# Kernel tuning notes

Measured on AMD Instinct MI355X. Metric: run time of the kernel, lower is better.

The kernel has to match this reference:

```python
import jax, jax.numpy as jnp
import numpy as np

DIM = 128
WS = 8            # window_size
NH = 4            # num_heads
SHIFT = 4         # shift_size
HD = DIM // NH    # head_dim = 32
SCALE = HD ** (-0.5)
N = WS * WS       # tokens per window = 64


def _rel_pos_index():
    # Static relative-position index, [N, N], values in [0, (2*WS-1)^2)
    coords = np.stack(np.meshgrid(np.arange(WS), np.arange(WS), indexing='ij'))  # [2,WS,WS]
    cf = coords.reshape(2, -1)                                                   # [2,N]
    rel = (cf[:, :, None] - cf[:, None, :]).transpose(1, 2, 0)                   # [N,N,2]
    rel[:, :, 0] += WS - 1
    rel[:, :, 1] += WS - 1
    rel[:, :, 0] *= 2 * WS - 1
    return rel.sum(-1)


def _shift_mask(H, W):
    # Static shifted-window attention mask, [nW, N, N] with 0 / -100 entries
    img = np.zeros((H, W))
    cnt = 0
    for hs in (slice(0, -WS), slice(-WS, -SHIFT), slice(-SHIFT, None)):
        for ws in (slice(0, -WS), slice(-WS, -SHIFT), slice(-SHIFT, None)):
            img[hs, ws] = cnt
            cnt += 1
    mw = img.reshape(H // WS, WS, W // WS, WS).transpose(0, 2, 1, 3).reshape(-1, N)
    am = mw[:, None, :] - mw[:, :, None]
    return np.where(am != 0, -100.0, 0.0).astype(np.float32)


def setup_inputs() -> dict:
    key = jax.random.key(0)
    ks = jax.random.split(key, 5)
    B, H, W = 8, 256, 256
    x = jax.random.normal(ks[0], (B, DIM, H, W), dtype=jnp.float32)
    qkv_w = jax.random.normal(ks[1], (3 * DIM, DIM), dtype=jnp.float32) * (DIM ** -0.5)
    proj_w = jax.random.normal(ks[2], (DIM, DIM), dtype=jnp.float32) * (DIM ** -0.5)
    proj_b = jax.random.normal(ks[3], (DIM,), dtype=jnp.float32) * 0.01
    bias_table = jax.random.normal(ks[4], ((2 * WS - 1) ** 2, NH), dtype=jnp.float32) * 0.02
    return {"x": x, "qkv_w": qkv_w, "proj_w": proj_w, "proj_b": proj_b,
            "bias_table": bias_table}


def reference(x, qkv_w, proj_w, proj_b, bias_table):
    B, C, H, W = x.shape
    # cyclic shift
    x = jnp.roll(x, (-SHIFT, -SHIFT), axis=(2, 3))
    # 1x1 conv qkv == channel matmul
    qkv = jnp.einsum('bchw,oc->bohw', x, qkv_w)  # [B, 3C, H, W]
    nWh, nWw = H // WS, W // WS
    nW = nWh * nWw
    qkv = qkv.reshape(B, 3, NH, HD, nWh, WS, nWw, WS)
    qkv = qkv.transpose(1, 0, 4, 6, 2, 5, 7, 3)          # [3,B,nWh,nWw,NH,WS,WS,HD]
    qkv = qkv.reshape(3, B * nW, NH, N, HD)
    q, k, v = qkv[0], qkv[1], qkv[2]
    attn = jnp.einsum('wnqd,wnkd->wnqk', q, k) * SCALE   # [B*nW, NH, N, N]
    # relative position bias gather
    rpi = _rel_pos_index().reshape(-1)
    bias = bias_table[rpi].reshape(N, N, NH).transpose(2, 0, 1)  # [NH,N,N]
    attn = attn + bias[None]
    # shifted-window mask
    mask = jnp.asarray(_shift_mask(H, W))                # [nW, N, N]
    attn = attn.reshape(B, nW, NH, N, N) + mask[None, :, None]
    attn = jax.nn.softmax(attn, axis=-1).reshape(B * nW, NH, N, N)
    out = jnp.einsum('wnqk,wnkd->wnqd', attn, v)         # [B*nW, NH, N, HD]
    out = out.reshape(B, nWh, nWw, NH, WS, WS, HD)
    out = out.transpose(0, 3, 6, 1, 4, 2, 5).reshape(B, C, H, W)
    out = jnp.einsum('bchw,oc->bohw', out, proj_w) + proj_b[None, :, None, None]
    out = jnp.roll(out, (SHIFT, SHIFT), axis=(2, 3))
    return out
```

## Files before the change

### kernel.cpp

```cpp
#include <hip/hip_runtime.h>

typedef __attribute__((ext_vector_type(8))) short short8;
typedef __attribute__((ext_vector_type(4))) unsigned short ushort4v;
typedef __attribute__((ext_vector_type(4))) float f32x4;

#define SCALE_F 0.17677669529663687f
#define SW(t) ((((t) ^ ((t) >> 3)) & 7) << 4)

__device__ __forceinline__ unsigned short f2bf(float f){
  unsigned u = __builtin_bit_cast(unsigned, f);
  u += 0x7fffu + ((u >> 16) & 1u);
  return (unsigned short)(u >> 16);
}
__device__ __forceinline__ float bf2f(unsigned short h){
  unsigned u = ((unsigned)h) << 16;
  return __builtin_bit_cast(float, u);
}
__device__ __forceinline__ unsigned cvtpk(float a, float b){
  unsigned w;
  asm("v_cvt_pk_bf16_f32 %0, %1, %2" : "=v"(w) : "v"(a), "v"(b));
  return w;
}
__device__ __forceinline__ void st_pk4(void* p, f32x4 a){
  uint2 u; u.x = cvtpk(a[0], a[1]); u.y = cvtpk(a[2], a[3]);
  *(uint2*)p = u;
}


template<bool WSB>
__global__ void __launch_bounds__(256, 2)
swin_fused(const float* __restrict__ x, const float* __restrict__ qkvw_f,
           const float* __restrict__ projw_f, const float* __restrict__ projb,
           const float* __restrict__ btab, const unsigned short* __restrict__ wbf,
           float* __restrict__ out)
{
  __shared__ __align__(16) unsigned char sm[65536];
  const int tid  = threadIdx.x;
  const int lane = tid & 63, wv = tid >> 6;
  const int lr = lane & 15, lg = lane >> 4;

  const int bid = blockIdx.x;
  const int sw  = ((bid & 7) << 10) | (bid >> 3);
  const int b   = sw >> 10;
  const int wh  = (sw >> 5) & 31, ww = sw & 31;
  const int hb  = wh * 8 + 4, wb = ww * 8 + 4;
  const bool h31 = (wh == 31), w31 = (ww == 31);

  short8 BwH[2][4];
  float pbH[2];
  #pragma unroll
  for (int ntl = 0; ntl < 2; ++ntl) {
    const int o = (wv + 4 * ntl) * 16 + lr;
    pbH[ntl] = projb[o];
    #pragma unroll
    for (int kk = 0; kk < 4; ++kk) {
      const int off = o * 128 + kk * 32 + 8 * lg;
      if constexpr (WSB) {
        BwH[ntl][kk] = *(const short8*)(wbf + 49152 + off);
      } else {
        const float* p = projw_f + off;
        short8 r;
        #pragma unroll
        for (int e = 0; e < 8; ++e) r[e] = (short)f2bf(p[e]);
        BwH[ntl][kk] = r;
      }
    }
  }

  {
    #pragma unroll
    for (int it = 0; it < 8; ++it) {
      const int f = tid + 256 * it;
      const int c    = f >> 4;
      const int rr   = (f >> 1) & 7;
      const int half = f & 1;
      const int gh = (hb + rr) & 255;
      const int gw = (wb + 4 * half) & 255;
      const f32x4 v = *(const f32x4*)(x + (((b * 128 + c) << 16) + (gh << 8) + gw));
      const int t0 = rr * 8 + 4 * half;
      #pragma unroll
      for (int e = 0; e < 4; ++e) {
        const int t = t0 + e;
        *(unsigned short*)(sm + t * 256 + ((2 * c) ^ SW(t))) = f2bf(v[e]);
      }
    }
  }
  __syncthreads();

  {
    short8 Bf[16];
    #pragma unroll
    for (int nt = 0; nt < 4; ++nt)
      #pragma unroll
      for (int kk = 0; kk < 4; ++kk) {
        const int t = nt * 16 + lr;
        Bf[nt * 4 + kk] = *(short8*)(sm + t * 256 + ((64 * kk + 16 * lg) ^ SW(t)));
      }
    #pragma unroll
    for (int jj = 0; jj < 6; ++jj) {
      const int mt = wv + 4 * jj;
      const int orow = mt * 16 + lr;
      short8 Af[4];
      #pragma unroll
      for (int kk = 0; kk < 4; ++kk) {
        const int off = orow * 128 + kk * 32 + 8 * lg;
        if constexpr (WSB) {
          Af[kk] = *(const short8*)(wbf + off);
        } else {
          const float* p = qkvw_f + off;
          short8 r;
          #pragma unroll
          for (int e = 0; e < 8; ++e) r[e] = (short)f2bf(p[e]);
          Af[kk] = r;
        }
      }
      f32x4 acc[4];
      #pragma unroll
      for (int nt = 0; nt < 4; ++nt) {
        acc[nt] = (f32x4)(0.f);
        #pragma unroll
        for (int kk = 0; kk < 4; ++kk)
          acc[nt] = __builtin_amdgcn_mfma_f32_16x16x32_bf16(Af[kk], Bf[nt * 4 + kk], acc[nt], 0, 0, 0);
      }
      if (mt < 16) {
        const int base = (mt < 8) ? 16384 : 32768;
        const int c0 = ((mt & 7) * 16) + 4 * lg;
        #pragma unroll
        for (int nt = 0; nt < 4; ++nt) {
          const int t = nt * 16 + lr;
          ushort4v pk;
          #pragma unroll
          for (int r = 0; r < 4; ++r) pk[r] = f2bf(acc[nt][r]);
          *(ushort4v*)(sm + base + t * 256 + ((2 * c0) ^ SW(t))) = pk;
        }
      } else {
        const int c0 = (mt - 16) * 16 + 4 * lg;
        #pragma unroll
        for (int nt = 0; nt < 4; ++nt) {
          const int t = nt * 16 + lr;
          #pragma unroll
          for (int r = 0; r < 4; ++r) {
            const int c = c0 + r;
            *(unsigned short*)(sm + 49152 + c * 128 + ((2 * t) ^ SW(c))) = f2bf(acc[nt][r]);
          }
        }
      }
    }
  }
  __syncthreads();

  const int ktc = wv * 16 + lr;
  const int ki = ktc >> 3, kj = ktc & 7;
  int boff[4][4];
  #pragma unroll
  for (int mt = 0; mt < 4; ++mt)
    #pragma unroll
    for (int r = 0; r < 4; ++r) {
      const int qrow = mt * 16 + 4 * lg + r;
      boff[mt][r] = (((qrow >> 3) - ki + 7) * 15 + ((qrow & 7) - kj + 7)) * 4;
    }

  f32x4 accpv[8];
  #pragma unroll
  for (int z = 0; z < 8; ++z) accpv[z] = (f32x4)(0.f);

  #pragma unroll 1
  for (int h = 0; h < 4; ++h) {
    {
      const int cb = 64 * h + 16 * lg;
      const short8 kb = *(short8*)(sm + 32768 + ktc * 256 + (cb ^ SW(ktc)));
      #pragma unroll
      for (int mt = 0; mt < 4; ++mt) {
        const int q = mt * 16 + lr;
        const short8 qa = *(short8*)(sm + 16384 + q * 256 + (cb ^ SW(q)));
        f32x4 sacc = __builtin_amdgcn_mfma_f32_16x16x32_bf16(qa, kb, (f32x4)(0.f), 0, 0, 0);
        #pragma unroll
        for (int r = 0; r < 4; ++r) {
          const int qrow = mt * 16 + 4 * lg + r;
          float s = sacc[r] * SCALE_F;
          s += btab[boff[mt][r] + h];
          if (h31 | w31) {
            const int qi = qrow >> 3, qj = qrow & 7;
            const bool bad = (h31 && ((qi >= 4) != (ki >= 4))) ||
                             (w31 && ((qj >= 4) != (kj >= 4)));
            s += bad ? -100.f : 0.f;
          }
          *(unsigned short*)(sm + qrow * 128 + ((2 * ktc) ^ SW(qrow))) = f2bf(s);
        }
      }
    }
    __syncthreads();
    {
      const int srow = tid >> 2, sq = tid & 3;
      const int swz = SW(srow);
      const short8 s0 = *(short8*)(sm + srow * 128 + ((sq * 32) ^ swz));
      const short8 s1 = *(short8*)(sm + srow * 128 + ((sq * 32 + 16) ^ swz));
      float v[16];
      #pragma unroll
      for (int e = 0; e < 8; ++e) { v[e] = bf2f((unsigned short)s0[e]); v[e + 8] = bf2f((unsigned short)s1[e]); }
      float mx = v[0];
      #pragma unroll
      for (int e = 1; e < 16; ++e) mx = fmaxf(mx, v[e]);
      mx = fmaxf(mx, __shfl_xor(mx, 1));
      mx = fmaxf(mx, __shfl_xor(mx, 2));
      float sum = 0.f;
      #pragma unroll
      for (int e = 0; e < 16; ++e) { v[e] = __expf(v[e] - mx); sum += v[e]; }
      sum += __shfl_xor(sum, 1);
      sum += __shfl_xor(sum, 2);
      const float inv = 1.f / sum;
      short8 p0, p1;
      #pragma unroll
      for (int e = 0; e < 8; ++e) { p0[e] = (short)f2bf(v[e] * inv); p1[e] = (short)f2bf(v[e + 8] * inv); }
      *(short8*)(sm + 8192 + srow * 128 + ((sq * 32) ^ swz)) = p0;
      *(short8*)(sm + 8192 + srow * 128 + ((sq * 32 + 16) ^ swz)) = p1;
    }
    __syncthreads();
    {
      const int q = wv * 16 + lr;
      const short8 pa0 = *(short8*)(sm + 8192 + q * 128 + ((16 * lg) ^ SW(q)));
      const short8 pa1 = *(short8*)(sm + 8192 + q * 128 + ((64 + 16 * lg) ^ SW(q)));
      #pragma unroll
      for (int nd = 0; nd < 2; ++nd) {
        const int c = h * 32 + nd * 16 + lr;
        const short8 vb0 = *(short8*)(sm + 49152 + c * 128 + ((16 * lg) ^ SW(c)));
        const short8 vb1 = *(short8*)(sm + 49152 + c * 128 + ((64 + 16 * lg) ^ SW(c)));
        f32x4 a = accpv[h * 2 + nd];
        a = __builtin_amdgcn_mfma_f32_16x16x32_bf16(pa0, vb0, a, 0, 0, 0);
        a = __builtin_amdgcn_mfma_f32_16x16x32_bf16(pa1, vb1, a, 0, 0, 0);
        accpv[h * 2 + nd] = a;
      }
    }
  }

  {
    #pragma unroll
    for (int h = 0; h < 4; ++h)
      #pragma unroll
      for (int nd = 0; nd < 2; ++nd) {
        const int c = h * 32 + nd * 16 + lr;
        const f32x4 a = accpv[h * 2 + nd];
        #pragma unroll
        for (int r = 0; r < 4; ++r) {
          const int t = wv * 16 + 4 * lg + r;
          *(unsigned short*)(sm + 16384 + t * 256 + ((2 * c) ^ SW(t))) = f2bf(a[r]);
        }
      }
  }
  __syncthreads();

  {
    short8 Aa[16];
    #pragma unroll
    for (int mt = 0; mt < 4; ++mt)
      #pragma unroll
      for (int kk = 0; kk < 4; ++kk) {
        const int t = mt * 16 + lr;
        Aa[mt * 4 + kk] = *(short8*)(sm + 16384 + t * 256 + ((64 * kk + 16 * lg) ^ SW(t)));
      }
    #pragma unroll
    for (int ntl = 0; ntl < 2; ++ntl) {
      const int o = (wv + 4 * ntl) * 16 + lr;
      const float pb = pbH[ntl];
      #pragma unroll
      for (int mt = 0; mt < 4; ++mt) {
        f32x4 acc = (f32x4)(0.f);
        #pragma unroll
        for (int kk = 0; kk < 4; ++kk)
          acc = __builtin_amdgcn_mfma_f32_16x16x32_bf16(Aa[mt * 4 + kk], BwH[ntl][kk], acc, 0, 0, 0);
        const int t0 = mt * 16 + 4 * lg;
        const int gh = (hb + (t0 >> 3)) & 255;
        const int gw0 = (wb + (t0 & 7)) & 255;
        f32x4 ov;
        ov[0] = acc[0] + pb; ov[1] = acc[1] + pb; ov[2] = acc[2] + pb; ov[3] = acc[3] + pb;
        *(f32x4*)(out + (((b * 128 + o) << 16) + (gh << 8) + gw0)) = ov;
      }
    }
  }
}

__global__ void prep_weights(const float* __restrict__ qw, const float* __restrict__ pw,
                             unsigned short* __restrict__ wsb)
{
  const int i = blockIdx.x * 256 + threadIdx.x;
  const int idx = i * 4;
  const float* src = (idx < 49152) ? (qw + idx) : (pw + (idx - 49152));
  f32x4 v = *(const f32x4*)src;
  ushort4v o;
  #pragma unroll
  for (int e = 0; e < 4; ++e) o[e] = f2bf(v[e]);
  *(ushort4v*)(wsb + idx) = o;
}

extern "C" void kernel_launch(void* const* d_in, const int* in_sizes, int n_in,
                              void* d_out, int out_size, void* d_ws, size_t ws_size,
                              hipStream_t stream) {
  const float* x     = (const float*)d_in[0];
  const float* qkvw  = (const float*)d_in[1];
  const float* projw = (const float*)d_in[2];
  const float* projb = (const float*)d_in[3];
  const float* btab  = (const float*)d_in[4];
  float* out = (float*)d_out;

  if (ws_size >= 131072) {
    unsigned short* wsb = (unsigned short*)d_ws;
    prep_weights<<<64, 256, 0, stream>>>(qkvw, projw, wsb);
    swin_fused<true><<<8192, 256, 0, stream>>>(x, qkvw, projw, projb, btab, wsb, out);
  } else {
    swin_fused<false><<<8192, 256, 0, stream>>>(x, qkvw, projw, projb, btab, nullptr, out);
  }
}
```

Baseline: 415.8 us.

## Double block to 512 threads, processing two heads in parallel per window

Raises threads per block from 256 to 512 so each window uses 8 waves. Work is split so that wave pairs handle two heads at once, each with its own score buffer, and the loop shrinks from four head iterations to two. The QKV and projection GEMMs are redistributed so each wave does fewer tiles. The softmax now writes probabilities in place with packed bf16 conversion, and the projection input is staged at a different LDS offset. This cuts per-wave serial work and register pressure, at the cost of an extra barrier per iteration. With 64KB LDS per block, occupancy stays limited to few blocks per CU.

```diff
diff --git a/kernel.cpp b/kernel.cpp
--- a/kernel.cpp
+++ b/kernel.cpp
@@ -21,14 +21,10 @@
   asm("v_cvt_pk_bf16_f32 %0, %1, %2" : "=v"(w) : "v"(a), "v"(b));
   return w;
 }
-__device__ __forceinline__ void st_pk4(void* p, f32x4 a){
-  uint2 u; u.x = cvtpk(a[0], a[1]); u.y = cvtpk(a[2], a[3]);
-  *(uint2*)p = u;
-}
 
 
 template<bool WSB>
-__global__ void __launch_bounds__(256, 2)
+__global__ void __launch_bounds__(512, 4)
 swin_fused(const float* __restrict__ x, const float* __restrict__ qkvw_f,
            const float* __restrict__ projw_f, const float* __restrict__ projb,
            const float* __restrict__ btab, const unsigned short* __restrict__ wbf,
@@ -46,31 +42,27 @@
   const int hb  = wh * 8 + 4, wb = ww * 8 + 4;
   const bool h31 = (wh == 31), w31 = (ww == 31);
 
-  short8 BwH[2][4];
-  float pbH[2];
+  short8 BwH[4];
+  const int oP = wv * 16 + lr;
+  const float pbH = projb[oP];
   #pragma unroll
-  for (int ntl = 0; ntl < 2; ++ntl) {
-    const int o = (wv + 4 * ntl) * 16 + lr;
-    pbH[ntl] = projb[o];
-    #pragma unroll
-    for (int kk = 0; kk < 4; ++kk) {
-      const int off = o * 128 + kk * 32 + 8 * lg;
-      if constexpr (WSB) {
-        BwH[ntl][kk] = *(const short8*)(wbf + 49152 + off);
-      } else {
-        const float* p = projw_f + off;
-        short8 r;
-        #pragma unroll
-        for (int e = 0; e < 8; ++e) r[e] = (short)f2bf(p[e]);
-        BwH[ntl][kk] = r;
-      }
+  for (int kk = 0; kk < 4; ++kk) {
+    const int off = oP * 128 + kk * 32 + 8 * lg;
+    if constexpr (WSB) {
+      BwH[kk] = *(const short8*)(wbf + 49152 + off);
+    } else {
+      const float* p = projw_f + off;
+      short8 r;
+      #pragma unroll
+      for (int e = 0; e < 8; ++e) r[e] = (short)f2bf(p[e]);
+      BwH[kk] = r;
     }
   }
 
   {
     #pragma unroll
-    for (int it = 0; it < 8; ++it) {
-      const int f = tid + 256 * it;
+    for (int it = 0; it < 4; ++it) {
+      const int f = tid + 512 * it;
       const int c    = f >> 4;
       const int rr   = (f >> 1) & 7;
       const int half = f & 1;
@@ -96,24 +88,24 @@
         const int t = nt * 16 + lr;
         Bf[nt * 4 + kk] = *(short8*)(sm + t * 256 + ((64 * kk + 16 * lg) ^ SW(t)));
       }
-    #pragma unroll
-    for (int jj = 0; jj < 6; ++jj) {
-      const int mt = wv + 4 * jj;
-      const int orow = mt * 16 + lr;
+    auto ldw = [&](int orow, int kk) -> short8 {
+      const int off = orow * 128 + kk * 32 + 8 * lg;
+      if constexpr (WSB) {
+        return *(const short8*)(wbf + off);
+      } else {
+        const float* p = qkvw_f + off;
+        short8 r;
+        #pragma unroll
+        for (int e = 0; e < 8; ++e) r[e] = (short)f2bf(p[e]);
+        return r;
+      }
+    };
+    #pragma unroll
+    for (int sec = 0; sec < 3; ++sec) {
+      const int orow = (8 * sec + wv) * 16 + lr;
       short8 Af[4];
       #pragma unroll
-      for (int kk = 0; kk < 4; ++kk) {
-        const int off = orow * 128 + kk * 32 + 8 * lg;
-        if constexpr (WSB) {
-          Af[kk] = *(const short8*)(wbf + off);
-        } else {
-          const float* p = qkvw_f + off;
-          short8 r;
-          #pragma unroll
-          for (int e = 0; e < 8; ++e) r[e] = (short)f2bf(p[e]);
-          Af[kk] = r;
-        }
-      }
+      for (int kk = 0; kk < 4; ++kk) Af[kk] = ldw(orow, kk);
       f32x4 acc[4];
       #pragma unroll
       for (int nt = 0; nt < 4; ++nt) {
@@ -122,9 +114,9 @@
         for (int kk = 0; kk < 4; ++kk)
           acc[nt] = __builtin_amdgcn_mfma_f32_16x16x32_bf16(Af[kk], Bf[nt * 4 + kk], acc[nt], 0, 0, 0);
       }
-      if (mt < 16) {
-        const int base = (mt < 8) ? 16384 : 32768;
-        const int c0 = ((mt & 7) * 16) + 4 * lg;
+      if (sec < 2) {
+        const int base = (sec == 0) ? 16384 : 32768;
+        const int c0 = wv * 16 + 4 * lg;
         #pragma unroll
         for (int nt = 0; nt < 4; ++nt) {
           const int t = nt * 16 + lr;
@@ -134,7 +126,7 @@
           *(ushort4v*)(sm + base + t * 256 + ((2 * c0) ^ SW(t))) = pk;
         }
       } else {
-        const int c0 = (mt - 16) * 16 + 4 * lg;
+        const int c0 = wv * 16 + 4 * lg;
         #pragma unroll
         for (int nt = 0; nt < 4; ++nt) {
           const int t = nt * 16 + lr;
@@ -149,7 +141,9 @@
   }
   __syncthreads();
 
-  const int ktc = wv * 16 + lr;
+  const int hpar = wv >> 2;
+  const int wt   = wv & 3;
+  const int ktc = wt * 16 + lr;
   const int ki = ktc >> 3, kj = ktc & 7;
   int boff[4][4];
   #pragma unroll
@@ -159,13 +153,15 @@
       const int qrow = mt * 16 + 4 * lg + r;
       boff[mt][r] = (((qrow >> 3) - ki + 7) * 15 + ((qrow & 7) - kj + 7)) * 4;
     }
-
-  f32x4 accpv[8];
+  const int Sbase = 8192 * hpar;
+
+  f32x4 accpv[4];
   #pragma unroll
-  for (int z = 0; z < 8; ++z) accpv[z] = (f32x4)(0.f);
+  for (int z = 0; z < 4; ++z) accpv[z] = (f32x4)(0.f);
 
   #pragma unroll 1
-  for (int h = 0; h < 4; ++h) {
+  for (int p = 0; p < 2; ++p) {
+    const int h = 2 * p + hpar;
     {
       const int cb = 64 * h + 16 * lg;
       const short8 kb = *(short8*)(sm + 32768 + ktc * 256 + (cb ^ SW(ktc)));
@@ -185,16 +181,20 @@
                              (w31 && ((qj >= 4) != (kj >= 4)));
             s += bad ? -100.f : 0.f;
           }
-          *(unsigned short*)(sm + qrow * 128 + ((2 * ktc) ^ SW(qrow))) = f2bf(s);
+          *(unsigned short*)(sm + Sbase + qrow * 128 + ((2 * ktc) ^ SW(qrow))) = f2bf(s);
         }
       }
     }
     __syncthreads();
     {
       const int srow = tid >> 2, sq = tid & 3;
-      const int swz = SW(srow);
-      const short8 s0 = *(short8*)(sm + srow * 128 + ((sq * 32) ^ swz));
-      const short8 s1 = *(short8*)(sm + srow * 128 + ((sq * 32 + 16) ^ swz));
+      const int rrow = srow & 63;
+      unsigned char* const rp = sm + (srow >> 6) * 8192 + rrow * 128;
+      const int swz = SW(rrow);
+      const int o0 = (sq * 32) ^ swz;
+      const int o1 = (sq * 32 + 16) ^ swz;
+      const short8 s0 = *(short8*)(rp + o0);
+      const short8 s1 = *(short8*)(rp + o1);
       float v[16];
       #pragma unroll
       for (int e = 0; e < 8; ++e) { v[e] = bf2f((unsigned short)s0[e]); v[e + 8] = bf2f((unsigned short)s1[e]); }
@@ -209,41 +209,47 @@
       sum += __shfl_xor(sum, 1);
       sum += __shfl_xor(sum, 2);
       const float inv = 1.f / sum;
-      short8 p0, p1;
-      #pragma unroll
-      for (int e = 0; e < 8; ++e) { p0[e] = (short)f2bf(v[e] * inv); p1[e] = (short)f2bf(v[e + 8] * inv); }
-      *(short8*)(sm + 8192 + srow * 128 + ((sq * 32) ^ swz)) = p0;
-      *(short8*)(sm + 8192 + srow * 128 + ((sq * 32 + 16) ^ swz)) = p1;
+      uint2 w0, w1;
+      w0.x = cvtpk(v[0] * inv,  v[1] * inv);  w0.y = cvtpk(v[2] * inv,  v[3] * inv);
+      w1.x = cvtpk(v[4] * inv,  v[5] * inv);  w1.y = cvtpk(v[6] * inv,  v[7] * inv);
+      *(uint2*)(rp + o0) = w0;
+      *(uint2*)(rp + o0 + 8) = w1;
+      uint2 w2, w3;
+      w2.x = cvtpk(v[8] * inv,  v[9] * inv);  w2.y = cvtpk(v[10] * inv, v[11] * inv);
+      w3.x = cvtpk(v[12] * inv, v[13] * inv); w3.y = cvtpk(v[14] * inv, v[15] * inv);
+      *(uint2*)(rp + o1) = w2;
+      *(uint2*)(rp + o1 + 8) = w3;
     }
     __syncthreads();
     {
-      const int q = wv * 16 + lr;
-      const short8 pa0 = *(short8*)(sm + 8192 + q * 128 + ((16 * lg) ^ SW(q)));
-      const short8 pa1 = *(short8*)(sm + 8192 + q * 128 + ((64 + 16 * lg) ^ SW(q)));
+      const int q = wt * 16 + lr;
+      const short8 pa0 = *(short8*)(sm + Sbase + q * 128 + ((16 * lg) ^ SW(q)));
+      const short8 pa1 = *(short8*)(sm + Sbase + q * 128 + ((64 + 16 * lg) ^ SW(q)));
       #pragma unroll
       for (int nd = 0; nd < 2; ++nd) {
-        const int c = h * 32 + nd * 16 + lr;
+        const int c = 32 * h + nd * 16 + lr;
         const short8 vb0 = *(short8*)(sm + 49152 + c * 128 + ((16 * lg) ^ SW(c)));
         const short8 vb1 = *(short8*)(sm + 49152 + c * 128 + ((64 + 16 * lg) ^ SW(c)));
-        f32x4 a = accpv[h * 2 + nd];
+        f32x4 a = accpv[2 * p + nd];
         a = __builtin_amdgcn_mfma_f32_16x16x32_bf16(pa0, vb0, a, 0, 0, 0);
         a = __builtin_amdgcn_mfma_f32_16x16x32_bf16(pa1, vb1, a, 0, 0, 0);
-        accpv[h * 2 + nd] = a;
-      }
-    }
+        accpv[2 * p + nd] = a;
+      }
+    }
+    __syncthreads();
   }
 
   {
     #pragma unroll
-    for (int h = 0; h < 4; ++h)
+    for (int p = 0; p < 2; ++p)
       #pragma unroll
       for (int nd = 0; nd < 2; ++nd) {
-        const int c = h * 32 + nd * 16 + lr;
-        const f32x4 a = accpv[h * 2 + nd];
+        const int c = 32 * (2 * p + hpar) + nd * 16 + lr;
+        const f32x4 a = accpv[2 * p + nd];
         #pragma unroll
         for (int r = 0; r < 4; ++r) {
-          const int t = wv * 16 + 4 * lg + r;
-          *(unsigned short*)(sm + 16384 + t * 256 + ((2 * c) ^ SW(t))) = f2bf(a[r]);
+          const int t = wt * 16 + 4 * lg + r;
+          *(unsigned short*)(sm + 49152 + t * 256 + ((2 * c) ^ SW(t))) = f2bf(a[r]);
         }
       }
   }
@@ -256,25 +262,20 @@
       #pragma unroll
       for (int kk = 0; kk < 4; ++kk) {
         const int t = mt * 16 + lr;
-        Aa[mt * 4 + kk] = *(short8*)(sm + 16384 + t * 256 + ((64 * kk + 16 * lg) ^ SW(t)));
-      }
-    #pragma unroll
-    for (int ntl = 0; ntl < 2; ++ntl) {
-      const int o = (wv + 4 * ntl) * 16 + lr;
-      const float pb = pbH[ntl];
-      #pragma unroll
-      for (int mt = 0; mt < 4; ++mt) {
-        f32x4 acc = (f32x4)(0.f);
-        #pragma unroll
-        for (int kk = 0; kk < 4; ++kk)
-          acc = __builtin_amdgcn_mfma_f32_16x16x32_bf16(Aa[mt * 4 + kk], BwH[ntl][kk], acc, 0, 0, 0);
-        const int t0 = mt * 16 + 4 * lg;
-        const int gh = (hb + (t0 >> 3)) & 255;
-        const int gw0 = (wb + (t0 & 7)) & 255;
-        f32x4 ov;
-        ov[0] = acc[0] + pb; ov[1] = acc[1] + pb; ov[2] = acc[2] + pb; ov[3] = acc[3] + pb;
-        *(f32x4*)(out + (((b * 128 + o) << 16) + (gh << 8) + gw0)) = ov;
-      }
+        Aa[mt * 4 + kk] = *(short8*)(sm + 49152 + t * 256 + ((64 * kk + 16 * lg) ^ SW(t)));
+      }
+    #pragma unroll
+    for (int mt = 0; mt < 4; ++mt) {
+      f32x4 acc = (f32x4)(0.f);
+      #pragma unroll
+      for (int kk = 0; kk < 4; ++kk)
+        acc = __builtin_amdgcn_mfma_f32_16x16x32_bf16(Aa[mt * 4 + kk], BwH[kk], acc, 0, 0, 0);
+      const int t0 = mt * 16 + 4 * lg;
+      const int gh = (hb + (t0 >> 3)) & 255;
+      const int gw0 = (wb + (t0 & 7)) & 255;
+      f32x4 ov;
+      ov[0] = acc[0] + pbH; ov[1] = acc[1] + pbH; ov[2] = acc[2] + pbH; ov[3] = acc[3] + pbH;
+      *(f32x4*)(out + (((b * 128 + oP) << 16) + (gh << 8) + gw0)) = ov;
     }
   }
 }
@@ -305,8 +306,8 @@
   if (ws_size >= 131072) {
     unsigned short* wsb = (unsigned short*)d_ws;
     prep_weights<<<64, 256, 0, stream>>>(qkvw, projw, wsb);
-    swin_fused<true><<<8192, 256, 0, stream>>>(x, qkvw, projw, projb, btab, wsb, out);
+    swin_fused<true><<<8192, 512, 0, stream>>>(x, qkvw, projw, projb, btab, wsb, out);
   } else {
-    swin_fused<false><<<8192, 256, 0, stream>>>(x, qkvw, projw, projb, btab, nullptr, out);
-  }
-}
+    swin_fused<false><<<8192, 512, 0, stream>>>(x, qkvw, projw, projb, btab, nullptr, out);
+  }
+}
```

Result: slower. 624.5 us (+50.2%).

## Split fused Swin attention into compute kernel plus coalesced output scatter kernel

Applied to the files above, without the earlier changes.

Adds a two-kernel path for when the workspace is large enough. The first kernel does the QKV projection, windowed attention and output projection using a smaller LDS footprint (about 39 KB, launch bounds for 4 blocks per CU). It writes bf16 results per window into scratch. The second kernel reads that scratch and writes full, coalesced fp32 output rows with the cyclic roll applied. The aim is higher occupancy and better-coalesced stores than the fused kernel, at the cost of an extra scratch write and read plus bf16 rounding of the output.

```diff
diff --git a/kernel.cpp b/kernel.cpp
--- a/kernel.cpp
+++ b/kernel.cpp
@@ -3,6 +3,7 @@
 typedef __attribute__((ext_vector_type(8))) short short8;
 typedef __attribute__((ext_vector_type(4))) unsigned short ushort4v;
 typedef __attribute__((ext_vector_type(4))) float f32x4;
+typedef __attribute__((ext_vector_type(4))) unsigned int uint4v;
 
 #define SCALE_F 0.17677669529663687f
 #define SW(t) ((((t) ^ ((t) >> 3)) & 7) << 4)
@@ -26,6 +27,259 @@
   *(uint2*)p = u;
 }
 
+__global__ void prep_weights(const float* __restrict__ qw, const float* __restrict__ pw,
+                             unsigned short* __restrict__ wsb)
+{
+  const int i = blockIdx.x * 256 + threadIdx.x;
+  const int idx = i * 4;
+  const float* src = (idx < 49152) ? (qw + idx) : (pw + (idx - 49152));
+  f32x4 v = *(const f32x4*)src;
+  ushort4v o;
+  #pragma unroll
+  for (int e = 0; e < 4; ++e) o[e] = f2bf(v[e]);
+  *(ushort4v*)(wsb + idx) = o;
+}
+
+__global__ void __launch_bounds__(256, 4)
+swin_k1(const float* __restrict__ x, const float* __restrict__ projb,
+        const float* __restrict__ btab, const unsigned short* __restrict__ wbf,
+        unsigned short* __restrict__ scr)
+{
+  __shared__ __align__(16) unsigned char sm[39424];
+  unsigned char* const smq = sm + 16384;
+  unsigned char* const smk = sm + 21504;
+  unsigned char* const smv = sm + 26624;
+  unsigned char* const smS = sm + 31232;
+
+  const int tid  = threadIdx.x;
+  const int lane = tid & 63, wv = tid >> 6;
+  const int lr = lane & 15, lg = lane >> 4;
+
+  const int bid = blockIdx.x;
+  const int sw  = ((bid & 7) << 10) | (bid >> 3);
+  const int b   = sw >> 10;
+  const int wh  = (sw >> 5) & 31, ww = sw & 31;
+  const int hb  = wh * 8 + 4, wb = ww * 8 + 4;
+  const bool h31 = (wh == 31), w31 = (ww == 31);
+  const int win = sw;
+
+  {
+    #pragma unroll
+    for (int it = 0; it < 8; ++it) {
+      const int f = tid + 256 * it;
+      const int c    = f >> 4;
+      const int rr   = (f >> 1) & 7;
+      const int half = f & 1;
+      const int gh = (hb + rr) & 255;
+      const int gw = (wb + 4 * half) & 255;
+      const f32x4 v = *(const f32x4*)(x + (((b * 128 + c) << 16) + (gh << 8) + gw));
+      const int t0 = rr * 8 + 4 * half;
+      #pragma unroll
+      for (int e = 0; e < 4; ++e) {
+        const int t = t0 + e;
+        *(unsigned short*)(sm + t * 256 + ((2 * c) ^ SW(t))) = f2bf(v[e]);
+      }
+    }
+  }
+  __syncthreads();
+
+  const int ktc = wv * 16 + lr;
+  const int ki = ktc >> 3, kj = ktc & 7;
+  int boff[4][4];
+  #pragma unroll
+  for (int mt = 0; mt < 4; ++mt)
+    #pragma unroll
+    for (int r = 0; r < 4; ++r) {
+      const int qrow = mt * 16 + 4 * lg + r;
+      boff[mt][r] = (((qrow >> 3) - ki + 7) * 15 + ((qrow & 7) - kj + 7)) * 4;
+    }
+
+  f32x4 accpv[8];
+  #pragma unroll
+  for (int z = 0; z < 8; ++z) accpv[z] = (f32x4)(0.f);
+
+  auto ldx = [&](int t, int kk) -> short8 {
+    return *(const short8*)(sm + t * 256 + ((64 * kk + 16 * lg) ^ SW(t)));
+  };
+  auto ldw8 = [&](int row, int kk) -> short8 {
+    return *(const short8*)(wbf + row * 128 + kk * 32 + 8 * lg);
+  };
+
+  #pragma unroll 1
+  for (int h = 0; h < 4; ++h) {
+    {
+      const int prow0 = ((wv < 2) ? 32 * h : 128 + 32 * h) + 16 * (wv & 1);
+      short8 Af[4];
+      #pragma unroll
+      for (int kk = 0; kk < 4; ++kk) Af[kk] = ldw8(prow0 + lr, kk);
+      unsigned char* const dst = (wv < 2) ? smq : smk;
+      #pragma unroll
+      for (int nt = 0; nt < 4; ++nt) {
+        const int t = nt * 16 + lr;
+        f32x4 acc = (f32x4)(0.f);
+        #pragma unroll
+        for (int kk = 0; kk < 4; ++kk)
+          acc = __builtin_amdgcn_mfma_f32_16x16x32_bf16(Af[kk], ldx(t, kk), acc, 0, 0, 0);
+        if (wv < 2) { acc[0] *= SCALE_F; acc[1] *= SCALE_F; acc[2] *= SCALE_F; acc[3] *= SCALE_F; }
+        st_pk4(dst + t * 80 + 32 * (wv & 1) + 8 * lg, acc);
+      }
+      const int vrow0 = 256 + 32 * h + 16 * (wv >> 1);
+      short8 Av[4];
+      #pragma unroll
+      for (int kk = 0; kk < 4; ++kk) Av[kk] = ldw8(vrow0 + lr, kk);
+      #pragma unroll
+      for (int ntl = 0; ntl < 2; ++ntl) {
+        const int t = (2 * (wv & 1) + ntl) * 16 + lr;
+        f32x4 acc = (f32x4)(0.f);
+        #pragma unroll
+        for (int kk = 0; kk < 4; ++kk)
+          acc = __builtin_amdgcn_mfma_f32_16x16x32_bf16(Av[kk], ldx(t, kk), acc, 0, 0, 0);
+        const int cb = 16 * (wv >> 1) + 4 * lg;
+        #pragma unroll
+        for (int r = 0; r < 4; ++r)
+          *(unsigned short*)(smv + (cb + r) * 144 + 2 * t) = f2bf(acc[r]);
+      }
+    }
+    __syncthreads();
+
+    {
+      const short8 kb = *(const short8*)(smk + ktc * 80 + 16 * lg);
+      #pragma unroll
+      for (int mt = 0; mt < 4; ++mt) {
+        const short8 qa = *(const short8*)(smq + (mt * 16 + lr) * 80 + 16 * lg);
+        const f32x4 s = __builtin_amdgcn_mfma_f32_16x16x32_bf16(qa, kb, (f32x4)(0.f), 0, 0, 0);
+        #pragma unroll
+        for (int r = 0; r < 4; ++r) {
+          const int qrow = mt * 16 + 4 * lg + r;
+          float val = s[r] + btab[boff[mt][r] + h];
+          if (h31 | w31) {
+            const int qi = qrow >> 3, qj = qrow & 7;
+            const bool bad = (h31 && ((qi >= 4) != (ki >= 4))) ||
+                             (w31 && ((qj >= 4) != (kj >= 4)));
+            val += bad ? -100.f : 0.f;
+          }
+          *(unsigned short*)(smS + qrow * 128 + ((2 * ktc) ^ SW(qrow))) = f2bf(val);
+        }
+      }
+    }
+    __syncthreads();
+
+    {
+      const int srow = tid >> 2, sq = tid & 3;
+      unsigned char* const rp = smS + srow * 128;
+      const int o0 = (32 * sq) ^ SW(srow);
+      const int o1 = (32 * sq + 16) ^ SW(srow);
+      const short8 s0 = *(const short8*)(rp + o0);
+      const short8 s1 = *(const short8*)(rp + o1);
+      float v[16];
+      #pragma unroll
+      for (int e = 0; e < 8; ++e) { v[e] = bf2f((unsigned short)s0[e]); v[e + 8] = bf2f((unsigned short)s1[e]); }
+      float mx = v[0];
+      #pragma unroll
+      for (int e = 1; e < 16; ++e) mx = fmaxf(mx, v[e]);
+      mx = fmaxf(mx, __shfl_xor(mx, 1));
+      mx = fmaxf(mx, __shfl_xor(mx, 2));
+      float sum = 0.f;
+      #pragma unroll
+      for (int e = 0; e < 16; ++e) { v[e] = __expf(v[e] - mx); sum += v[e]; }
+      sum += __shfl_xor(sum, 1);
+      sum += __shfl_xor(sum, 2);
+      const float inv = 1.f / sum;
+      uint4v w0, w1;
+      w0.x = cvtpk(v[0] * inv, v[1] * inv);  w0.y = cvtpk(v[2] * inv, v[3] * inv);
+      w0.z = cvtpk(v[4] * inv, v[5] * inv);  w0.w = cvtpk(v[6] * inv, v[7] * inv);
+      w1.x = cvtpk(v[8] * inv, v[9] * inv);  w1.y = cvtpk(v[10] * inv, v[11] * inv);
+      w1.z = cvtpk(v[12] * inv, v[13] * inv); w1.w = cvtpk(v[14] * inv, v[15] * inv);
+      *(uint4v*)(rp + o0) = w0;
+      *(uint4v*)(rp + o1) = w1;
+    }
+    __syncthreads();
+
+    {
+      const int q = wv * 16 + lr;
+      const short8 pa0 = *(const short8*)(smS + q * 128 + ((16 * lg) ^ SW(q)));
+      const short8 pa1 = *(const short8*)(smS + q * 128 + ((64 + 16 * lg) ^ SW(q)));
+      #pragma unroll
+      for (int nd = 0; nd < 2; ++nd) {
+        const int c = nd * 16 + lr;
+        const short8 vb0 = *(const short8*)(smv + c * 144 + 16 * lg);
+        const short8 vb1 = *(const short8*)(smv + c * 144 + 64 + 16 * lg);
+        f32x4 a = accpv[2 * h + nd];
+        a = __builtin_amdgcn_mfma_f32_16x16x32_bf16(pa0, vb0, a, 0, 0, 0);
+        a = __builtin_amdgcn_mfma_f32_16x16x32_bf16(pa1, vb1, a, 0, 0, 0);
+        accpv[2 * h + nd] = a;
+      }
+    }
+    __syncthreads();
+  }
+
+  {
+    #pragma unroll
+    for (int h = 0; h < 4; ++h)
+      #pragma unroll
+      for (int nd = 0; nd < 2; ++nd) {
+        const int c = 32 * h + nd * 16 + lr;
+        const f32x4 a = accpv[2 * h + nd];
+        #pragma unroll
+        for (int r = 0; r < 4; ++r) {
+          const int t = wv * 16 + 4 * lg + r;
+          *(unsigned short*)(sm + t * 256 + ((2 * c) ^ SW(t))) = f2bf(a[r]);
+        }
+      }
+  }
+  __syncthreads();
+
+  {
+    short8 Aa[16];
+    #pragma unroll
+    for (int mt = 0; mt < 4; ++mt)
+      #pragma unroll
+      for (int kk = 0; kk < 4; ++kk) {
+        const int t = mt * 16 + lr;
+        Aa[mt * 4 + kk] = *(const short8*)(sm + t * 256 + ((64 * kk + 16 * lg) ^ SW(t)));
+      }
+    #pragma unroll
+    for (int ntl = 0; ntl < 2; ++ntl) {
+      const int o = (wv + 4 * ntl) * 16 + lr;
+      short8 Bw[4];
+      #pragma unroll
+      for (int kk = 0; kk < 4; ++kk)
+        Bw[kk] = *(const short8*)(wbf + 49152 + o * 128 + kk * 32 + 8 * lg);
+      const float pb = projb[o];
+      #pragma unroll
+      for (int mt = 0; mt < 4; ++mt) {
+        f32x4 acc = (f32x4)(0.f);
+        #pragma unroll
+        for (int kk = 0; kk < 4; ++kk)
+          acc = __builtin_amdgcn_mfma_f32_16x16x32_bf16(Aa[mt * 4 + kk], Bw[kk], acc, 0, 0, 0);
+        const int t0 = mt * 16 + 4 * lg;
+        uint2 u;
+        u.x = cvtpk(acc[0] + pb, acc[1] + pb);
+        u.y = cvtpk(acc[2] + pb, acc[3] + pb);
+        *(uint2*)(scr + ((win * 128 + o) << 6) + t0) = u;
+      }
+    }
+  }
+}
+
+__global__ void __launch_bounds__(256, 8)
+swin_k2(const unsigned short* __restrict__ scr, float* __restrict__ out)
+{
+  const int bid = blockIdx.x;
+  const int b = bid >> 12, whp = (bid >> 7) & 31, o = bid & 127;
+  const int tid = threadIdx.x;
+  const int gl = tid >> 5, l32 = tid & 31;
+  const int win = b * 1024 + whp * 32 + l32;
+  const short8 u = *(const short8*)(scr + ((win * 128 + o) << 6) + (gl << 3));
+  const int gh = (whp * 8 + 4 + gl) & 255;
+  float* const orow = out + (((b * 128 + o) << 16) + (gh << 8));
+  f32x4 v0, v1;
+  #pragma unroll
+  for (int e = 0; e < 4; ++e) { v0[e] = bf2f((unsigned short)u[e]); v1[e] = bf2f((unsigned short)u[e + 4]); }
+  const int gw0 = 8 * l32 + 4;
+  *(f32x4*)(orow + gw0) = v0;
+  *(f32x4*)(orow + ((gw0 + 4) & 255)) = v1;
+}
 
 template<bool WSB>
 __global__ void __launch_bounds__(256, 2)
@@ -279,19 +533,6 @@
   }
 }
 
-__global__ void prep_weights(const float* __restrict__ qw, const float* __restrict__ pw,
-                             unsigned short* __restrict__ wsb)
-{
-  const int i = blockIdx.x * 256 + threadIdx.x;
-  const int idx = i * 4;
-  const float* src = (idx < 49152) ? (qw + idx) : (pw + (idx - 49152));
-  f32x4 v = *(const f32x4*)src;
-  ushort4v o;
-  #pragma unroll
-  for (int e = 0; e < 4; ++e) o[e] = f2bf(v[e]);
-  *(ushort4v*)(wsb + idx) = o;
-}
-
 extern "C" void kernel_launch(void* const* d_in, const int* in_sizes, int n_in,
                               void* d_out, int out_size, void* d_ws, size_t ws_size,
                               hipStream_t stream) {
@@ -302,7 +543,14 @@
   const float* btab  = (const float*)d_in[4];
   float* out = (float*)d_out;
 
-  if (ws_size >= 131072) {
+  const size_t need_split = 131072u + (size_t)8192 * 8192 * 2;
+  if (ws_size >= need_split) {
+    unsigned short* wsb = (unsigned short*)d_ws;
+    unsigned short* scr = wsb + 65536;
+    prep_weights<<<64, 256, 0, stream>>>(qkvw, projw, wsb);
+    swin_k1<<<8192, 256, 0, stream>>>(x, projb, btab, wsb, scr);
+    swin_k2<<<32768, 256, 0, stream>>>(scr, out);
+  } else if (ws_size >= 131072) {
     unsigned short* wsb = (unsigned short*)d_ws;
     prep_weights<<<64, 256, 0, stream>>>(qkvw, projw, wsb);
     swin_fused<true><<<8192, 256, 0, stream>>>(x, qkvw, projw, projb, btab, wsb, out);
```

Result: slower. 561.5 us (+35.1%).

## Precompute dense bf16 bias table, defer proj weight loads, simplify LDS swizzle

Applied to the files above, without the earlier changes.

Adds a prep kernel that expands the relative-position bias into a dense bf16 [NH,64,64] table in workspace, so the attention loop reads bias by direct index instead of keeping a 16-entry offset array and doing a gather. Projection weights and bias are now loaded just before the output GEMM rather than held in registers for the whole kernel, which lowers register pressure. The LDS swizzle is simplified to use only the low row bits, and the head loop loses its no-unroll pragma. Risks: the new swizzle may cause more bank conflicts, bias values get bf16 rounding, and the workspace requirement grows.

```diff
diff --git a/kernel.cpp b/kernel.cpp
--- a/kernel.cpp
+++ b/kernel.cpp
@@ -5,7 +5,7 @@
 typedef __attribute__((ext_vector_type(4))) float f32x4;
 
 #define SCALE_F 0.17677669529663687f
-#define SW(t) ((((t) ^ ((t) >> 3)) & 7) << 4)
+#define SW(t) (((t) & 7) << 4)
 
 __device__ __forceinline__ unsigned short f2bf(float f){
   unsigned u = __builtin_bit_cast(unsigned, f);
@@ -16,16 +16,27 @@
   unsigned u = ((unsigned)h) << 16;
   return __builtin_bit_cast(float, u);
 }
-__device__ __forceinline__ unsigned cvtpk(float a, float b){
-  unsigned w;
-  asm("v_cvt_pk_bf16_f32 %0, %1, %2" : "=v"(w) : "v"(a), "v"(b));
-  return w;
-}
-__device__ __forceinline__ void st_pk4(void* p, f32x4 a){
-  uint2 u; u.x = cvtpk(a[0], a[1]); u.y = cvtpk(a[2], a[3]);
-  *(uint2*)p = u;
-}
-
+
+__global__ void prep_weights(const float* __restrict__ qw, const float* __restrict__ pw,
+                             unsigned short* __restrict__ wsb)
+{
+  const int i = blockIdx.x * 256 + threadIdx.x;
+  const int idx = i * 4;
+  const float* src = (idx < 49152) ? (qw + idx) : (pw + (idx - 49152));
+  f32x4 v = *(const f32x4*)src;
+  ushort4v o;
+  #pragma unroll
+  for (int e = 0; e < 4; ++e) o[e] = f2bf(v[e]);
+  *(ushort4v*)(wsb + idx) = o;
+}
+
+__global__ void prep_bias(const float* __restrict__ btab, unsigned short* __restrict__ biasb)
+{
+  const int idx = blockIdx.x * 256 + threadIdx.x;
+  const int h = idx >> 12, q = (idx >> 6) & 63, k = idx & 63;
+  const int rpi = ((q >> 3) - (k >> 3) + 7) * 15 + ((q & 7) - (k & 7) + 7);
+  biasb[idx] = f2bf(btab[rpi * 4 + h]);
+}
 
 template<bool WSB>
 __global__ void __launch_bounds__(256, 2)
@@ -46,27 +57,6 @@
   const int hb  = wh * 8 + 4, wb = ww * 8 + 4;
   const bool h31 = (wh == 31), w31 = (ww == 31);
 
-  short8 BwH[2][4];
-  float pbH[2];
-  #pragma unroll
-  for (int ntl = 0; ntl < 2; ++ntl) {
-    const int o = (wv + 4 * ntl) * 16 + lr;
-    pbH[ntl] = projb[o];
-    #pragma unroll
-    for (int kk = 0; kk < 4; ++kk) {
-      const int off = o * 128 + kk * 32 + 8 * lg;
-      if constexpr (WSB) {
-        BwH[ntl][kk] = *(const short8*)(wbf + 49152 + off);
-      } else {
-        const float* p = projw_f + off;
-        short8 r;
-        #pragma unroll
-        for (int e = 0; e < 8; ++e) r[e] = (short)f2bf(p[e]);
-        BwH[ntl][kk] = r;
-      }
-    }
-  }
-
   {
     #pragma unroll
     for (int it = 0; it < 8; ++it) {
@@ -152,19 +142,21 @@
   const int ktc = wv * 16 + lr;
   const int ki = ktc >> 3, kj = ktc & 7;
   int boff[4][4];
-  #pragma unroll
-  for (int mt = 0; mt < 4; ++mt)
-    #pragma unroll
-    for (int r = 0; r < 4; ++r) {
-      const int qrow = mt * 16 + 4 * lg + r;
-      boff[mt][r] = (((qrow >> 3) - ki + 7) * 15 + ((qrow & 7) - kj + 7)) * 4;
-    }
+  if constexpr (!WSB) {
+    #pragma unroll
+    for (int mt = 0; mt < 4; ++mt)
+      #pragma unroll
+      for (int r = 0; r < 4; ++r) {
+        const int qrow = mt * 16 + 4 * lg + r;
+        boff[mt][r] = (((qrow >> 3) - ki + 7) * 15 + ((qrow & 7) - kj + 7)) * 4;
+      }
+  }
+  const unsigned short* const biasb = WSB ? (wbf + 65536) : nullptr;
 
   f32x4 accpv[8];
   #pragma unroll
   for (int z = 0; z < 8; ++z) accpv[z] = (f32x4)(0.f);
 
-  #pragma unroll 1
   for (int h = 0; h < 4; ++h) {
     {
       const int cb = 64 * h + 16 * lg;
@@ -178,7 +170,11 @@
         for (int r = 0; r < 4; ++r) {
           const int qrow = mt * 16 + 4 * lg + r;
           float s = sacc[r] * SCALE_F;
-          s += btab[boff[mt][r] + h];
+          if constexpr (WSB) {
+            s += bf2f(biasb[(h << 12) | (qrow << 6) | ktc]);
+          } else {
+            s += btab[boff[mt][r] + h];
+          }
           if (h31 | w31) {
             const int qi = qrow >> 3, qj = qrow & 7;
             const bool bad = (h31 && ((qi >= 4) != (ki >= 4))) ||
@@ -261,13 +257,27 @@
     #pragma unroll
     for (int ntl = 0; ntl < 2; ++ntl) {
       const int o = (wv + 4 * ntl) * 16 + lr;
-      const float pb = pbH[ntl];
+      short8 Bw[4];
+      #pragma unroll
+      for (int kk = 0; kk < 4; ++kk) {
+        const int off = o * 128 + kk * 32 + 8 * lg;
+        if constexpr (WSB) {
+          Bw[kk] = *(const short8*)(wbf + 49152 + off);
+        } else {
+          const float* p = projw_f + off;
+          short8 r;
+          #pragma unroll
+          for (int e = 0; e < 8; ++e) r[e] = (short)f2bf(p[e]);
+          Bw[kk] = r;
+        }
+      }
+      const float pb = projb[o];
       #pragma unroll
       for (int mt = 0; mt < 4; ++mt) {
         f32x4 acc = (f32x4)(0.f);
         #pragma unroll
         for (int kk = 0; kk < 4; ++kk)
-          acc = __builtin_amdgcn_mfma_f32_16x16x32_bf16(Aa[mt * 4 + kk], BwH[ntl][kk], acc, 0, 0, 0);
+          acc = __builtin_amdgcn_mfma_f32_16x16x32_bf16(Aa[mt * 4 + kk], Bw[kk], acc, 0, 0, 0);
         const int t0 = mt * 16 + 4 * lg;
         const int gh = (hb + (t0 >> 3)) & 255;
         const int gw0 = (wb + (t0 & 7)) & 255;
@@ -277,19 +287,6 @@
       }
     }
   }
-}
-
-__global__ void prep_weights(const float* __restrict__ qw, const float* __restrict__ pw,
-                             unsigned short* __restrict__ wsb)
-{
-  const int i = blockIdx.x * 256 + threadIdx.x;
-  const int idx = i * 4;
-  const float* src = (idx < 49152) ? (qw + idx) : (pw + (idx - 49152));
-  f32x4 v = *(const f32x4*)src;
-  ushort4v o;
-  #pragma unroll
-  for (int e = 0; e < 4; ++e) o[e] = f2bf(v[e]);
-  *(ushort4v*)(wsb + idx) = o;
 }
 
 extern "C" void kernel_launch(void* const* d_in, const int* in_sizes, int n_in,
@@ -302,9 +299,10 @@
   const float* btab  = (const float*)d_in[4];
   float* out = (float*)d_out;
 
-  if (ws_size >= 131072) {
+  if (ws_size >= 163840) {
     unsigned short* wsb = (unsigned short*)d_ws;
     prep_weights<<<64, 256, 0, stream>>>(qkvw, projw, wsb);
+    prep_bias<<<64, 256, 0, stream>>>(btab, wsb + 65536);
     swin_fused<true><<<8192, 256, 0, stream>>>(x, qkvw, projw, projb, btab, wsb, out);
   } else {
     swin_fused<false><<<8192, 256, 0, stream>>>(x, qkvw, projw, projb, btab, nullptr, out);
```

After: 559.1 us. 1.34x slower.
